# Kernel optimization log

Measured on AMD Instinct MI355X. Metric: run time of the kernel, lower is better.

Reference implementation:

```python
import jax, jax.numpy as jnp
import numpy as np

H = 8  # GRU hidden size (Dimension)


def _gru_last_hidden(x, Wih, Whh, bih, bhh):
    """Torch-style GRU (batch_first), returns final hidden state [B, H].
    x: [B, T, In]; Wih: [3H, In]; Whh: [3H, H]; bih, bhh: [3H].
    Gate order (torch): r, z, n.
    """
    B = x.shape[0]
    # precompute input projections for all timesteps: [B, T, 3H]
    xg = jnp.einsum('bti,gi->btg', x, Wih) + bih

    def step(h, xt):  # h: [B,H], xt: [B,3H]
        gh = h @ Whh.T + bhh  # [B, 3H]
        xr, xz, xn = jnp.split(xt, 3, axis=-1)
        hr, hz, hn = jnp.split(gh, 3, axis=-1)
        r = jax.nn.sigmoid(xr + hr)
        z = jax.nn.sigmoid(xz + hz)
        n = jnp.tanh(xn + r * hn)
        h_new = (1.0 - z) * n + z * h
        return h_new, None

    h0 = jnp.zeros((B, H), dtype=x.dtype)
    hT, _ = jax.lax.scan(step, h0, jnp.swapaxes(xg, 0, 1))  # scan over T
    return hT


def setup_inputs() -> dict:
    key = jax.random.key(0)
    ks = jax.random.split(key, 10)
    B, T = 1024, 512
    s = 0.2  # param init scale ~ 1/sqrt(H)*... small
    return {
        'bbox': jax.random.normal(ks[0], (B, T, 4), dtype=jnp.float32),
        'flow': jax.random.normal(ks[1], (B, T, 5, 5, 2), dtype=jnp.float32),
        'Wih_b': jax.random.normal(ks[2], (3 * H, 4), dtype=jnp.float32) * s,
        'Whh_b': jax.random.normal(ks[3], (3 * H, H), dtype=jnp.float32) * s,
        'bih_b': jax.random.normal(ks[4], (3 * H,), dtype=jnp.float32) * s,
        'bhh_b': jax.random.normal(ks[5], (3 * H,), dtype=jnp.float32) * s,
        'Wih_f': jax.random.normal(ks[6], (3 * H, 2), dtype=jnp.float32) * s,
        'Whh_f': jax.random.normal(ks[7], (3 * H, H), dtype=jnp.float32) * s,
        'bih_f': jax.random.normal(ks[8], (3 * H,), dtype=jnp.float32) * s,
        'bhh_f': jax.random.normal(ks[9], (3 * H,), dtype=jnp.float32) * s,
    }


def reference(bbox, flow, Wih_b, Whh_b, bih_b, bhh_b, Wih_f, Whh_f, bih_f, bhh_f):
    # vectorized equivalent of the triple Python loop: take center pixel
    storage = flow[:, :, 2, 2, :]  # [B, T, 2]
    h_bbox = _gru_last_hidden(bbox, Wih_b, Whh_b, bih_b, bhh_b)      # [B, H]
    h_flow = _gru_last_hidden(storage, Wih_f, Whh_f, bih_f, bhh_f)   # [B, H]
    feature = (h_bbox + h_flow) * 0.5
    return feature
```

## Files before the change

kernel.cpp:

```cpp
#include <hip/hip_runtime.h>

#define HDIM 8

__device__ __forceinline__ float ex2(float x) {
#if __has_builtin(__builtin_amdgcn_exp2f)
    return __builtin_amdgcn_exp2f(x);
#else
    return exp2f(x);
#endif
}
__device__ __forceinline__ float rcp(float x) {
#if __has_builtin(__builtin_amdgcn_rcpf)
    return __builtin_amdgcn_rcpf(x);
#else
    return 1.0f / x;
#endif
}

#define DPP_ROR(v, N)                                                        \
    __int_as_float(__builtin_amdgcn_update_dpp(                              \
        0, __float_as_int(v), 0x120 + (N), 0xF, 0xF, true))

template <int IN, int STRIDE>
__device__ float gru_elem(const float* __restrict__ xbase, int T,
                          const float* __restrict__ Wih, const float* __restrict__ Whh,
                          const float* __restrict__ bih, const float* __restrict__ bhh,
                          int j)
{
    const float NL2E = -1.4426950408889634f;
    const float L2E2 =  2.8853900817779268f;

    float nbp = DPP_ROR((float)j, 2);
    const int dstep = (nbp == (float)((j + 1) & 7)) ? 1 : 7;

    float wr[8], wz[8], wn[8];
#pragma unroll
    for (int m = 0; m < 8; ++m) {
        const int k = (j + dstep * m) & 7;
        wr[m] = NL2E * Whh[(j     ) * HDIM + k];
        wz[m] = NL2E * Whh[(j +  8) * HDIM + k];
        wn[m] = L2E2 * Whh[(j + 16) * HDIM + k];
    }
    float uir[IN], uiz[IN], uin[IN];
#pragma unroll
    for (int i = 0; i < IN; ++i) {
        uir[i] = NL2E * Wih[(j     ) * IN + i];
        uiz[i] = NL2E * Wih[(j +  8) * IN + i];
        uin[i] = L2E2 * Wih[(j + 16) * IN + i];
    }
    const float br  = NL2E * (bih[j]     + bhh[j]);
    const float bz  = NL2E * (bih[j + 8] + bhh[j + 8]);
    const float bn  = L2E2 * bih[j + 16];
    const float bhn = L2E2 * bhh[j + 16];

    constexpr int U = 8;
    float xb[U][IN];
    float pr[U], pz[U], pn[U];

    auto loadx = [&](const float* px) {
#pragma unroll
        for (int s = 0; s < U; ++s) {
            const float* p = px + s * STRIDE;
            if constexpr (IN == 4) {
                float4 v = *reinterpret_cast<const float4*>(p);
                xb[s][0] = v.x; xb[s][1] = v.y; xb[s][2] = v.z; xb[s][3] = v.w;
            } else {
                float2 v = *reinterpret_cast<const float2*>(p);
                xb[s][0] = v.x; xb[s][1] = v.y;
            }
        }
    };
    auto proj = [&]() {
#pragma unroll
        for (int s = 0; s < U; ++s) {
            float a = br, b = bz, c = bn;
#pragma unroll
            for (int i = 0; i < IN; ++i) {
                a = fmaf(uir[i], xb[s][i], a);
                b = fmaf(uiz[i], xb[s][i], b);
                c = fmaf(uin[i], xb[s][i], c);
            }
            pr[s] = a; pz[s] = b; pn[s] = c;
        }
    };

    const float* px = xbase;
    loadx(px);
    proj();
    px += U * STRIDE;
    float hj = 0.0f;

    for (int t0 = 0; t0 < T; t0 += U) {
        if (t0 + U < T) {
            loadx(px);
            px += U * STRIDE;
        }
#pragma unroll
        for (int s = 0; s < U; ++s) {
            const float hx0 = hj;
            const float hx1 = DPP_ROR(hj,  2);
            const float hx2 = DPP_ROR(hj,  4);
            const float hx3 = DPP_ROR(hj,  6);
            const float hx4 = DPP_ROR(hj,  8);
            const float hx5 = DPP_ROR(hj, 10);
            const float hx6 = DPP_ROR(hj, 12);
            const float hx7 = DPP_ROR(hj, 14);

            float ra = fmaf(wr[3], hx3, fmaf(wr[2], hx2, fmaf(wr[1], hx1, fmaf(wr[0], hx0, pr[s]))));
            float rb = fmaf(wr[7], hx7, fmaf(wr[6], hx6, fmaf(wr[5], hx5, wr[4] * hx4)));
            float za = fmaf(wz[3], hx3, fmaf(wz[2], hx2, fmaf(wz[1], hx1, fmaf(wz[0], hx0, pz[s]))));
            float zb = fmaf(wz[7], hx7, fmaf(wz[6], hx6, fmaf(wz[5], hx5, wz[4] * hx4)));
            float na = fmaf(wn[3], hx3, fmaf(wn[2], hx2, fmaf(wn[1], hx1, fmaf(wn[0], hx0, bhn))));
            float nb2 = fmaf(wn[7], hx7, fmaf(wn[6], hx6, fmaf(wn[5], hx5, wn[4] * hx4)));
            float sr = ra + rb;
            float sz = za + zb;
            float sn = na + nb2;

            float r = rcp(1.0f + ex2(sr));
            float z = rcp(1.0f + ex2(sz));
            float u = fmaf(r, sn, pn[s]);
            float n = fmaf(-2.0f, rcp(1.0f + ex2(u)), 1.0f);
            hj = fmaf(z, hj - n, n);
        }
        proj();
    }
    return hj;
}

__global__ __launch_bounds__(128, 1)
void gru_fused_kernel(const float* __restrict__ bbox, const float* __restrict__ flow,
                      const float* __restrict__ Wih_b, const float* __restrict__ Whh_b,
                      const float* __restrict__ bih_b, const float* __restrict__ bhh_b,
                      const float* __restrict__ Wih_f, const float* __restrict__ Whh_f,
                      const float* __restrict__ bih_f, const float* __restrict__ bhh_f,
                      float* __restrict__ out, int T)
{
    const int tid   = threadIdx.x;
    const int wave  = tid >> 6;
    const int lane  = tid & 63;
    const int eloc  = ((lane >> 4) << 1) | (lane & 1);
    const int j     = (lane & 15) >> 1;
    const int e     = blockIdx.x * 8 + eloc;

    __shared__ float sh[2][8][HDIM];

    float hT;
    if (wave == 0) {
        const float* xb = bbox + (size_t)e * T * 4;
        hT = gru_elem<4, 4>(xb, T, Wih_b, Whh_b, bih_b, bhh_b, j);
    } else {
        const float* xf = flow + (size_t)e * T * 50 + 24;
        hT = gru_elem<2, 50>(xf, T, Wih_f, Whh_f, bih_f, bhh_f, j);
    }

    sh[wave][eloc][j] = hT;
    __syncthreads();
    if (wave == 0) {
        out[(size_t)e * HDIM + j] = 0.5f * (sh[0][eloc][j] + sh[1][eloc][j]);
    }
}

extern "C" void kernel_launch(void* const* d_in, const int* in_sizes, int n_in,
                              void* d_out, int out_size, void* d_ws, size_t ws_size,
                              hipStream_t stream) {
    const float* bbox  = (const float*)d_in[0];
    const float* flow  = (const float*)d_in[1];
    const float* Wih_b = (const float*)d_in[2];
    const float* Whh_b = (const float*)d_in[3];
    const float* bih_b = (const float*)d_in[4];
    const float* bhh_b = (const float*)d_in[5];
    const float* Wih_f = (const float*)d_in[6];
    const float* Whh_f = (const float*)d_in[7];
    const float* bih_f = (const float*)d_in[8];
    const float* bhh_f = (const float*)d_in[9];
    float* out = (float*)d_out;

    const int B = out_size / HDIM;
    const int T = in_sizes[0] / (4 * B);

    dim3 grid(B / 8), block(128);
    gru_fused_kernel<<<grid, block, 0, stream>>>(
        bbox, flow, Wih_b, Whh_b, bih_b, bhh_b,
        Wih_f, Whh_f, bih_f, bhh_f, out, T);
}
```

Measured before the change: 68.62 us.

## Split GRU into producer waves for input projections and consumer waves for recurrence

Adds two producer waves per block that load the inputs and compute the input-gate projections for chunks of 16 timesteps. They write these into double-buffered LDS, and the two consumer waves read them while running the serial recurrence. The aim is to take global-memory latency and projection math off the recurrence's critical path. The trade-offs are a block barrier every chunk, twice as many threads per block, and extra LDS traffic. The code also assumes T is divisible by the chunk size.

```diff
diff --git a/kernel.cpp b/kernel.cpp
--- a/kernel.cpp
+++ b/kernel.cpp
@@ -1,6 +1,7 @@
 #include <hip/hip_runtime.h>
 
 #define HDIM 8
+#define CHUNK 16
 
 __device__ __forceinline__ float ex2(float x) {
 #if __has_builtin(__builtin_amdgcn_exp2f)
@@ -21,113 +22,90 @@
     __int_as_float(__builtin_amdgcn_update_dpp(                              \
         0, __float_as_int(v), 0x120 + (N), 0xF, 0xF, true))
 
+
 template <int IN, int STRIDE>
-__device__ float gru_elem(const float* __restrict__ xbase, int T,
-                          const float* __restrict__ Wih, const float* __restrict__ Whh,
-                          const float* __restrict__ bih, const float* __restrict__ bhh,
-                          int j)
+__device__ __forceinline__ void produce_chunk(
+    const float* __restrict__ xb, int t0,
+    const float (&uir)[8][4], const float (&uiz)[8][4], const float (&uin)[8][4],
+    const float (&cr)[8], const float (&cz)[8], const float (&cn)[8],
+    float* dst, int el, int q)
 {
-    const float NL2E = -1.4426950408889634f;
-    const float L2E2 =  2.8853900817779268f;
-
-    float nbp = DPP_ROR((float)j, 2);
-    const int dstep = (nbp == (float)((j + 1) & 7)) ? 1 : 7;
-
-    float wr[8], wz[8], wn[8];
-#pragma unroll
-    for (int m = 0; m < 8; ++m) {
-        const int k = (j + dstep * m) & 7;
-        wr[m] = NL2E * Whh[(j     ) * HDIM + k];
-        wz[m] = NL2E * Whh[(j +  8) * HDIM + k];
-        wn[m] = L2E2 * Whh[(j + 16) * HDIM + k];
-    }
-    float uir[IN], uiz[IN], uin[IN];
-#pragma unroll
-    for (int i = 0; i < IN; ++i) {
-        uir[i] = NL2E * Wih[(j     ) * IN + i];
-        uiz[i] = NL2E * Wih[(j +  8) * IN + i];
-        uin[i] = L2E2 * Wih[(j + 16) * IN + i];
-    }
-    const float br  = NL2E * (bih[j]     + bhh[j]);
-    const float bz  = NL2E * (bih[j + 8] + bhh[j + 8]);
-    const float bn  = L2E2 * bih[j + 16];
-    const float bhn = L2E2 * bhh[j + 16];
-
-    constexpr int U = 8;
-    float xb[U][IN];
-    float pr[U], pz[U], pn[U];
-
-    auto loadx = [&](const float* px) {
-#pragma unroll
-        for (int s = 0; s < U; ++s) {
-            const float* p = px + s * STRIDE;
-            if constexpr (IN == 4) {
-                float4 v = *reinterpret_cast<const float4*>(p);
-                xb[s][0] = v.x; xb[s][1] = v.y; xb[s][2] = v.z; xb[s][3] = v.w;
-            } else {
-                float2 v = *reinterpret_cast<const float2*>(p);
-                xb[s][0] = v.x; xb[s][1] = v.y;
+#pragma unroll
+    for (int h = 0; h < 2; ++h) {
+        const int s = q + 8 * h;
+        const float* p = xb + (size_t)(t0 + s) * STRIDE;
+        float x[IN];
+        if constexpr (IN == 4) {
+            float4 v = *reinterpret_cast<const float4*>(p);
+            x[0] = v.x; x[1] = v.y; x[2] = v.z; x[3] = v.w;
+        } else {
+            float2 v = *reinterpret_cast<const float2*>(p);
+            x[0] = v.x; x[1] = v.y;
+        }
+#pragma unroll
+        for (int jj = 0; jj < 8; ++jj) {
+            float a = cr[jj], b = cz[jj], c = cn[jj];
+#pragma unroll
+            for (int i = 0; i < IN; ++i) {
+                a = fmaf(uir[jj][i], x[i], a);
+                b = fmaf(uiz[jj][i], x[i], b);
+                c = fmaf(uin[jj][i], x[i], c);
             }
-        }
-    };
-    auto proj = [&]() {
-#pragma unroll
-        for (int s = 0; s < U; ++s) {
-            float a = br, b = bz, c = bn;
-#pragma unroll
-            for (int i = 0; i < IN; ++i) {
-                a = fmaf(uir[i], xb[s][i], a);
-                b = fmaf(uiz[i], xb[s][i], b);
-                c = fmaf(uin[i], xb[s][i], c);
-            }
-            pr[s] = a; pz[s] = b; pn[s] = c;
-        }
-    };
-
-    const float* px = xbase;
-    loadx(px);
-    proj();
-    px += U * STRIDE;
-    float hj = 0.0f;
-
-    for (int t0 = 0; t0 < T; t0 += U) {
-        if (t0 + U < T) {
-            loadx(px);
-            px += U * STRIDE;
-        }
-#pragma unroll
-        for (int s = 0; s < U; ++s) {
-            const float hx0 = hj;
-            const float hx1 = DPP_ROR(hj,  2);
-            const float hx2 = DPP_ROR(hj,  4);
-            const float hx3 = DPP_ROR(hj,  6);
-            const float hx4 = DPP_ROR(hj,  8);
-            const float hx5 = DPP_ROR(hj, 10);
-            const float hx6 = DPP_ROR(hj, 12);
-            const float hx7 = DPP_ROR(hj, 14);
-
-            float ra = fmaf(wr[3], hx3, fmaf(wr[2], hx2, fmaf(wr[1], hx1, fmaf(wr[0], hx0, pr[s]))));
-            float rb = fmaf(wr[7], hx7, fmaf(wr[6], hx6, fmaf(wr[5], hx5, wr[4] * hx4)));
-            float za = fmaf(wz[3], hx3, fmaf(wz[2], hx2, fmaf(wz[1], hx1, fmaf(wz[0], hx0, pz[s]))));
-            float zb = fmaf(wz[7], hx7, fmaf(wz[6], hx6, fmaf(wz[5], hx5, wz[4] * hx4)));
-            float na = fmaf(wn[3], hx3, fmaf(wn[2], hx2, fmaf(wn[1], hx1, fmaf(wn[0], hx0, bhn))));
-            float nb2 = fmaf(wn[7], hx7, fmaf(wn[6], hx6, fmaf(wn[5], hx5, wn[4] * hx4)));
-            float sr = ra + rb;
-            float sz = za + zb;
-            float sn = na + nb2;
-
-            float r = rcp(1.0f + ex2(sr));
-            float z = rcp(1.0f + ex2(sz));
-            float u = fmaf(r, sn, pn[s]);
-            float n = fmaf(-2.0f, rcp(1.0f + ex2(u)), 1.0f);
-            hj = fmaf(z, hj - n, n);
-        }
-        proj();
+            *reinterpret_cast<float4*>(dst + (size_t)(s * 8 + el) * 32 + jj * 4)
+                = make_float4(a, b, c, 0.0f);
+        }
+    }
+}
+
+__device__ __forceinline__ float consume_chunk(
+    float hj, const float* __restrict__ src, int el, int j,
+    const float (&wr)[8], const float (&wz)[8], const float (&wn)[8], float bhn)
+{
+    float4 pf[3];
+    pf[0] = *reinterpret_cast<const float4*>(src + (size_t)(0 * 8 + el) * 32 + j * 4);
+    pf[1] = *reinterpret_cast<const float4*>(src + (size_t)(1 * 8 + el) * 32 + j * 4);
+#pragma unroll
+    for (int s = 0; s < CHUNK; ++s) {
+        if (s + 2 < CHUNK)
+            pf[(s + 2) % 3] = *reinterpret_cast<const float4*>(
+                src + (size_t)((s + 2) * 8 + el) * 32 + j * 4);
+        const float4 P = pf[s % 3];
+
+        const float hx0 = hj;
+        const float hx1 = DPP_ROR(hj,  2);
+        const float hx2 = DPP_ROR(hj,  4);
+        const float hx3 = DPP_ROR(hj,  6);
+        const float hx4 = DPP_ROR(hj,  8);
+        const float hx5 = DPP_ROR(hj, 10);
+        const float hx6 = DPP_ROR(hj, 12);
+        const float hx7 = DPP_ROR(hj, 14);
+
+        float r01 = fmaf(wr[1], hx1, fmaf(wr[0], hx0, P.x));
+        float r23 = fmaf(wr[3], hx3, wr[2] * hx2);
+        float r45 = fmaf(wr[5], hx5, wr[4] * hx4);
+        float r67 = fmaf(wr[7], hx7, wr[6] * hx6);
+        float z01 = fmaf(wz[1], hx1, fmaf(wz[0], hx0, P.y));
+        float z23 = fmaf(wz[3], hx3, wz[2] * hx2);
+        float z45 = fmaf(wz[5], hx5, wz[4] * hx4);
+        float z67 = fmaf(wz[7], hx7, wz[6] * hx6);
+        float n01 = fmaf(wn[1], hx1, fmaf(wn[0], hx0, bhn));
+        float n23 = fmaf(wn[3], hx3, wn[2] * hx2);
+        float n45 = fmaf(wn[5], hx5, wn[4] * hx4);
+        float n67 = fmaf(wn[7], hx7, wn[6] * hx6);
+        float sr = (r01 + r23) + (r45 + r67);
+        float sz = (z01 + z23) + (z45 + z67);
+        float sn = (n01 + n23) + (n45 + n67);
+
+        float r = rcp(1.0f + ex2(sr));
+        float z = rcp(1.0f + ex2(sz));
+        float u = fmaf(r, sn, P.z);
+        float n = fmaf(-2.0f, rcp(1.0f + ex2(u)), 1.0f);
+        hj = fmaf(z, hj - n, n);
     }
     return hj;
 }
 
-__global__ __launch_bounds__(128, 1)
+__global__ __launch_bounds__(256, 1)
 void gru_fused_kernel(const float* __restrict__ bbox, const float* __restrict__ flow,
                       const float* __restrict__ Wih_b, const float* __restrict__ Whh_b,
                       const float* __restrict__ bih_b, const float* __restrict__ bhh_b,
@@ -135,27 +113,88 @@
                       const float* __restrict__ bih_f, const float* __restrict__ bhh_f,
                       float* __restrict__ out, int T)
 {
-    const int tid   = threadIdx.x;
-    const int wave  = tid >> 6;
-    const int lane  = tid & 63;
-    const int eloc  = ((lane >> 4) << 1) | (lane & 1);
-    const int j     = (lane & 15) >> 1;
-    const int e     = blockIdx.x * 8 + eloc;
-
+    const float NL2E = -1.4426950408889634f;
+    const float L2E2 =  2.8853900817779268f;
+
+    __shared__ float projLDS[2][2][CHUNK][8][32];
     __shared__ float sh[2][8][HDIM];
 
-    float hT;
-    if (wave == 0) {
-        const float* xb = bbox + (size_t)e * T * 4;
-        hT = gru_elem<4, 4>(xb, T, Wih_b, Whh_b, bih_b, bhh_b, j);
+    const int tid  = threadIdx.x;
+    const int wave = tid >> 6;
+    const int lane = tid & 63;
+    const int gru  = wave & 1;
+    const bool is_cons = (wave < 2);
+    const int NC = T / CHUNK;
+
+    const int eloc = ((lane >> 4) << 1) | (lane & 1);
+    const int j    = (lane & 15) >> 1;
+    float wr[8], wz[8], wn[8];
+    float bhn = 0.0f;
+
+    float uir[8][4], uiz[8][4], uin[8][4], cr[8], cz[8], cn[8];
+    const float* pxb = nullptr;
+    const int pel = lane >> 3;
+    const int pq  = lane & 7;
+
+    if (is_cons) {
+        const float* Whh = gru ? Whh_f : Whh_b;
+        const float* bhh = gru ? bhh_f : bhh_b;
+        float nbp = DPP_ROR((float)j, 2);
+        const int dstep = (nbp == (float)((j + 1) & 7)) ? 1 : 7;
+#pragma unroll
+        for (int m = 0; m < 8; ++m) {
+            const int k = (j + dstep * m) & 7;
+            wr[m] = NL2E * Whh[(j     ) * HDIM + k];
+            wz[m] = NL2E * Whh[(j +  8) * HDIM + k];
+            wn[m] = L2E2 * Whh[(j + 16) * HDIM + k];
+        }
+        bhn = L2E2 * bhh[j + 16];
     } else {
-        const float* xf = flow + (size_t)e * T * 50 + 24;
-        hT = gru_elem<2, 50>(xf, T, Wih_f, Whh_f, bih_f, bhh_f, j);
-    }
-
-    sh[wave][eloc][j] = hT;
+        const float* Wih = gru ? Wih_f : Wih_b;
+        const float* bih = gru ? bih_f : bih_b;
+        const float* bhh = gru ? bhh_f : bhh_b;
+        const int IN = gru ? 2 : 4;
+        const int pe = blockIdx.x * 8 + pel;
+        pxb = gru ? (flow + (size_t)pe * T * 50 + 24)
+                  : (bbox + (size_t)pe * T * 4);
+#pragma unroll
+        for (int jj = 0; jj < 8; ++jj) {
+            for (int i = 0; i < 4; ++i) { uir[jj][i] = 0.f; uiz[jj][i] = 0.f; uin[jj][i] = 0.f; }
+            for (int i = 0; i < IN; ++i) {
+                uir[jj][i] = NL2E * Wih[(jj     ) * IN + i];
+                uiz[jj][i] = NL2E * Wih[(jj +  8) * IN + i];
+                uin[jj][i] = L2E2 * Wih[(jj + 16) * IN + i];
+            }
+            cr[jj] = NL2E * (bih[jj]     + bhh[jj]);
+            cz[jj] = NL2E * (bih[jj + 8] + bhh[jj + 8]);
+            cn[jj] = L2E2 * bih[jj + 16];
+        }
+    }
+
+    float hj = 0.0f;
+
+    if (!is_cons) {
+        float* dst = &projLDS[0][gru][0][0][0];
+        if (gru == 0) produce_chunk<4, 4 >(pxb, 0, uir, uiz, uin, cr, cz, cn, dst, pel, pq);
+        else          produce_chunk<2, 50>(pxb, 0, uir, uiz, uin, cr, cz, cn, dst, pel, pq);
+    }
+    __syncthreads();
+
+    for (int c = 0; c < NC; ++c) {
+        if (is_cons) {
+            hj = consume_chunk(hj, &projLDS[c & 1][gru][0][0][0], eloc, j, wr, wz, wn, bhn);
+        } else if (c + 1 < NC) {
+            float* dst = &projLDS[(c + 1) & 1][gru][0][0][0];
+            if (gru == 0) produce_chunk<4, 4 >(pxb, (c + 1) * CHUNK, uir, uiz, uin, cr, cz, cn, dst, pel, pq);
+            else          produce_chunk<2, 50>(pxb, (c + 1) * CHUNK, uir, uiz, uin, cr, cz, cn, dst, pel, pq);
+        }
+        __syncthreads();
+    }
+
+    if (is_cons) sh[gru][eloc][j] = hj;
     __syncthreads();
     if (wave == 0) {
+        const int e = blockIdx.x * 8 + eloc;
         out[(size_t)e * HDIM + j] = 0.5f * (sh[0][eloc][j] + sh[1][eloc][j]);
     }
 }
@@ -178,7 +217,7 @@
     const int B = out_size / HDIM;
     const int T = in_sizes[0] / (4 * B);
 
-    dim3 grid(B / 8), block(128);
+    dim3 grid(B / 8), block(256);
     gru_fused_kernel<<<grid, block, 0, stream>>>(
         bbox, flow, Wih_b, Whh_b, bih_b, bhh_b,
         Wih_f, Whh_f, bih_f, bhh_f, out, T);
```

After: 81.18 us. 18.3% more time.

## Fuse DPP rotations into FMAs via inline asm and reorder gate math

Applied to the files above, without the earlier changes.

Replaces the separate DPP move plus FMA per hidden-state neighbour with v_mul_f32_dpp and v_fmac_f32_dpp inline asm, removing the extra move instructions on the serial recurrence critical path. The gate computation is reordered so the r gate's exp starts early, and the final blend is algebraically rewritten to shorten the dependency chain. Input loads become double-buffered A/B register sets with a 16-step loop, and the input projection is computed per step instead of batched. Weight setup is hoisted out of the templated body. The volatile asm limits compiler scheduling, and the loop assumes T is a multiple of 16.

```diff
diff --git a/kernel.cpp b/kernel.cpp
--- a/kernel.cpp
+++ b/kernel.cpp
@@ -1,6 +1,10 @@
 #include <hip/hip_runtime.h>
+#include <type_traits>
 
 #define HDIM 8
+
+typedef float v4f __attribute__((ext_vector_type(4)));
+typedef float v2f __attribute__((ext_vector_type(2)));
 
 __device__ __forceinline__ float ex2(float x) {
 #if __has_builtin(__builtin_amdgcn_exp2f)
@@ -21,108 +25,116 @@
     __int_as_float(__builtin_amdgcn_update_dpp(                              \
         0, __float_as_int(v), 0x120 + (N), 0xF, 0xF, true))
 
+#define ASM_FMA(d, a, b, c)                                                  \
+    asm volatile("v_fma_f32 %0, %1, %2, %3"                                  \
+                 : "=v"(d) : "v"(a), "v"(b), "v"(c))
+#define ASM_MULD(d, h, w, ROT)                                               \
+    asm volatile("v_mul_f32_dpp %0, %1, %2 row_ror:" #ROT                    \
+                 " row_mask:0xf bank_mask:0xf"                               \
+                 : "=v"(d) : "v"(h), "v"(w))
+#define ASM_FMACD(d, h, w, ROT)                                              \
+    asm volatile("v_fmac_f32_dpp %0, %1, %2 row_ror:" #ROT                   \
+                 " row_mask:0xf bank_mask:0xf"                               \
+                 : "+v"(d) : "v"(h), "v"(w))
+
+#define MEMBAR asm volatile("" ::: "memory")
+
+__device__ __forceinline__ float gru_step(float hj, v4f P,
+    const float (&wr)[8], const float (&wz)[8], const float (&wn)[8], float bhn)
+{
+    float ra, rb, na, nb, za, zb;
+    ASM_FMA (ra, wr[0], hj, P.x);
+    ASM_FMA (na, wn[0], hj, bhn);
+    ASM_MULD(rb, hj, wr[4], 8);
+    ASM_MULD(nb, hj, wn[4], 8);
+    ASM_FMACD(ra, hj, wr[1], 2);   ASM_FMACD(na, hj, wn[1], 2);
+    ASM_FMACD(rb, hj, wr[5], 10);  ASM_FMACD(nb, hj, wn[5], 10);
+    ASM_FMACD(ra, hj, wr[2], 4);   ASM_FMACD(na, hj, wn[2], 4);
+    ASM_FMACD(rb, hj, wr[6], 12);  ASM_FMACD(nb, hj, wn[6], 12);
+    ASM_FMACD(ra, hj, wr[3], 6);   ASM_FMACD(na, hj, wn[3], 6);
+    ASM_FMACD(rb, hj, wr[7], 14);  ASM_FMACD(nb, hj, wn[7], 14);
+    const float ar = ra + rb;
+    const float Er = ex2(ar);
+    ASM_FMA (za, wz[0], hj, P.y);
+    ASM_MULD(zb, hj, wz[4], 8);
+    ASM_FMACD(za, hj, wz[1], 2);
+    ASM_FMACD(zb, hj, wz[5], 10);
+    ASM_FMACD(za, hj, wz[2], 4);
+    ASM_FMACD(zb, hj, wz[6], 12);
+    ASM_FMACD(za, hj, wz[3], 6);
+    ASM_FMACD(zb, hj, wz[7], 14);
+    const float an_ = na + nb;
+    const float r  = rcp(1.0f + Er);
+    const float az = za + zb;
+    const float Ez = ex2(az);
+    const float u  = fmaf(r, an_, P.z);
+    const float En = ex2(u);
+    const float z  = rcp(1.0f + Ez);
+    const float q   = z * hj;
+    const float oz  = Ez * z;
+    const float s1  = q + oz;
+    const float m2o = -2.0f * oz;
+    const float rn  = rcp(1.0f + En);
+    return fmaf(rn, m2o, s1);
+}
+
 template <int IN, int STRIDE>
-__device__ float gru_elem(const float* __restrict__ xbase, int T,
-                          const float* __restrict__ Wih, const float* __restrict__ Whh,
-                          const float* __restrict__ bih, const float* __restrict__ bhh,
-                          int j)
+__device__ __forceinline__ float gru_run(
+    const float* __restrict__ px, int T,
+    const float (&ur)[4], const float (&uz)[4], const float (&un)[4],
+    float cr, float cz, float cn,
+    const float (&wr)[8], const float (&wz)[8], const float (&wn)[8], float bhn)
 {
-    const float NL2E = -1.4426950408889634f;
-    const float L2E2 =  2.8853900817779268f;
-
-    float nbp = DPP_ROR((float)j, 2);
-    const int dstep = (nbp == (float)((j + 1) & 7)) ? 1 : 7;
-
-    float wr[8], wz[8], wn[8];
+    using vx = std::conditional_t<IN == 4, v4f, v2f>;
+    auto LD = [&](int t) -> vx {
+        return *reinterpret_cast<const vx*>(px + (size_t)t * STRIDE);
+    };
+    auto PROJ = [&](vx x) -> v4f {
+        float a = cr, b = cz, c = cn;
 #pragma unroll
-    for (int m = 0; m < 8; ++m) {
-        const int k = (j + dstep * m) & 7;
-        wr[m] = NL2E * Whh[(j     ) * HDIM + k];
-        wz[m] = NL2E * Whh[(j +  8) * HDIM + k];
-        wn[m] = L2E2 * Whh[(j + 16) * HDIM + k];
-    }
-    float uir[IN], uiz[IN], uin[IN];
-#pragma unroll
-    for (int i = 0; i < IN; ++i) {
-        uir[i] = NL2E * Wih[(j     ) * IN + i];
-        uiz[i] = NL2E * Wih[(j +  8) * IN + i];
-        uin[i] = L2E2 * Wih[(j + 16) * IN + i];
-    }
-    const float br  = NL2E * (bih[j]     + bhh[j]);
-    const float bz  = NL2E * (bih[j + 8] + bhh[j + 8]);
-    const float bn  = L2E2 * bih[j + 16];
-    const float bhn = L2E2 * bhh[j + 16];
-
-    constexpr int U = 8;
-    float xb[U][IN];
-    float pr[U], pz[U], pn[U];
-
-    auto loadx = [&](const float* px) {
-#pragma unroll
-        for (int s = 0; s < U; ++s) {
-            const float* p = px + s * STRIDE;
-            if constexpr (IN == 4) {
-                float4 v = *reinterpret_cast<const float4*>(p);
-                xb[s][0] = v.x; xb[s][1] = v.y; xb[s][2] = v.z; xb[s][3] = v.w;
-            } else {
-                float2 v = *reinterpret_cast<const float2*>(p);
-                xb[s][0] = v.x; xb[s][1] = v.y;
-            }
+        for (int i = 0; i < IN; ++i) {
+            a = fmaf(ur[i], x[i], a);
+            b = fmaf(uz[i], x[i], b);
+            c = fmaf(un[i], x[i], c);
         }
+        return v4f{a, b, c, 0.0f};
     };
-    auto proj = [&]() {
-#pragma unroll
-        for (int s = 0; s < U; ++s) {
-            float a = br, b = bz, c = bn;
-#pragma unroll
-            for (int i = 0; i < IN; ++i) {
-                a = fmaf(uir[i], xb[s][i], a);
-                b = fmaf(uiz[i], xb[s][i], b);
-                c = fmaf(uin[i], xb[s][i], c);
-            }
-            pr[s] = a; pz[s] = b; pn[s] = c;
+
+    vx A0, A1, A2, A3, A4, A5, A6, A7;
+    vx B0, B1, B2, B3, B4, B5, B6, B7;
+
+    A0 = LD(0); A1 = LD(1); A2 = LD(2); A3 = LD(3);
+    A4 = LD(4); A5 = LD(5); A6 = LD(6); A7 = LD(7);
+    MEMBAR;
+
+    float hj = 0.0f;
+    for (int t0 = 0; t0 < T; t0 += 16) {
+        if (t0 + 8 < T) {
+            B0 = LD(t0 + 8);  B1 = LD(t0 + 9);  B2 = LD(t0 + 10); B3 = LD(t0 + 11);
+            B4 = LD(t0 + 12); B5 = LD(t0 + 13); B6 = LD(t0 + 14); B7 = LD(t0 + 15);
         }
-    };
-
-    const float* px = xbase;
-    loadx(px);
-    proj();
-    px += U * STRIDE;
-    float hj = 0.0f;
-
-    for (int t0 = 0; t0 < T; t0 += U) {
-        if (t0 + U < T) {
-            loadx(px);
-            px += U * STRIDE;
+        MEMBAR;
+        hj = gru_step(hj, PROJ(A0), wr, wz, wn, bhn);
+        hj = gru_step(hj, PROJ(A1), wr, wz, wn, bhn);
+        hj = gru_step(hj, PROJ(A2), wr, wz, wn, bhn);
+        hj = gru_step(hj, PROJ(A3), wr, wz, wn, bhn);
+        hj = gru_step(hj, PROJ(A4), wr, wz, wn, bhn);
+        hj = gru_step(hj, PROJ(A5), wr, wz, wn, bhn);
+        hj = gru_step(hj, PROJ(A6), wr, wz, wn, bhn);
+        hj = gru_step(hj, PROJ(A7), wr, wz, wn, bhn);
+        if (t0 + 16 < T) {
+            A0 = LD(t0 + 16); A1 = LD(t0 + 17); A2 = LD(t0 + 18); A3 = LD(t0 + 19);
+            A4 = LD(t0 + 20); A5 = LD(t0 + 21); A6 = LD(t0 + 22); A7 = LD(t0 + 23);
         }
-#pragma unroll
-        for (int s = 0; s < U; ++s) {
-            const float hx0 = hj;
-            const float hx1 = DPP_ROR(hj,  2);
-            const float hx2 = DPP_ROR(hj,  4);
-            const float hx3 = DPP_ROR(hj,  6);
-            const float hx4 = DPP_ROR(hj,  8);
-            const float hx5 = DPP_ROR(hj, 10);
-            const float hx6 = DPP_ROR(hj, 12);
-            const float hx7 = DPP_ROR(hj, 14);
-
-            float ra = fmaf(wr[3], hx3, fmaf(wr[2], hx2, fmaf(wr[1], hx1, fmaf(wr[0], hx0, pr[s]))));
-            float rb = fmaf(wr[7], hx7, fmaf(wr[6], hx6, fmaf(wr[5], hx5, wr[4] * hx4)));
-            float za = fmaf(wz[3], hx3, fmaf(wz[2], hx2, fmaf(wz[1], hx1, fmaf(wz[0], hx0, pz[s]))));
-            float zb = fmaf(wz[7], hx7, fmaf(wz[6], hx6, fmaf(wz[5], hx5, wz[4] * hx4)));
-            float na = fmaf(wn[3], hx3, fmaf(wn[2], hx2, fmaf(wn[1], hx1, fmaf(wn[0], hx0, bhn))));
-            float nb2 = fmaf(wn[7], hx7, fmaf(wn[6], hx6, fmaf(wn[5], hx5, wn[4] * hx4)));
-            float sr = ra + rb;
-            float sz = za + zb;
-            float sn = na + nb2;
-
-            float r = rcp(1.0f + ex2(sr));
-            float z = rcp(1.0f + ex2(sz));
-            float u = fmaf(r, sn, pn[s]);
-            float n = fmaf(-2.0f, rcp(1.0f + ex2(u)), 1.0f);
-            hj = fmaf(z, hj - n, n);
-        }
-        proj();
+        MEMBAR;
+        hj = gru_step(hj, PROJ(B0), wr, wz, wn, bhn);
+        hj = gru_step(hj, PROJ(B1), wr, wz, wn, bhn);
+        hj = gru_step(hj, PROJ(B2), wr, wz, wn, bhn);
+        hj = gru_step(hj, PROJ(B3), wr, wz, wn, bhn);
+        hj = gru_step(hj, PROJ(B4), wr, wz, wn, bhn);
+        hj = gru_step(hj, PROJ(B5), wr, wz, wn, bhn);
+        hj = gru_step(hj, PROJ(B6), wr, wz, wn, bhn);
+        hj = gru_step(hj, PROJ(B7), wr, wz, wn, bhn);
     }
     return hj;
 }
@@ -135,22 +147,54 @@
                       const float* __restrict__ bih_f, const float* __restrict__ bhh_f,
                       float* __restrict__ out, int T)
 {
-    const int tid   = threadIdx.x;
-    const int wave  = tid >> 6;
-    const int lane  = tid & 63;
-    const int eloc  = ((lane >> 4) << 1) | (lane & 1);
-    const int j     = (lane & 15) >> 1;
-    const int e     = blockIdx.x * 8 + eloc;
+    const float NL2E = -1.4426950408889634f;
+    const float L2E2 =  2.8853900817779268f;
 
     __shared__ float sh[2][8][HDIM];
+
+    const int tid  = threadIdx.x;
+    const int wave = tid >> 6;
+    const int lane = tid & 63;
+    const int eloc = ((lane >> 4) << 1) | (lane & 1);
+    const int j    = (lane & 15) >> 1;
+    const int e    = blockIdx.x * 8 + eloc;
+
+    const float* Wih = wave ? Wih_f : Wih_b;
+    const float* Whh = wave ? Whh_f : Whh_b;
+    const float* bih = wave ? bih_f : bih_b;
+    const float* bhh = wave ? bhh_f : bhh_b;
+    const int IN = wave ? 2 : 4;
+
+    float nbp = DPP_ROR((float)j, 2);
+    const int dstep = (nbp == (float)((j + 1) & 7)) ? 1 : 7;
+
+    float wr[8], wz[8], wn[8];
+#pragma unroll
+    for (int m = 0; m < 8; ++m) {
+        const int k = (j + dstep * m) & 7;
+        wr[m] = NL2E * Whh[(j     ) * HDIM + k];
+        wz[m] = NL2E * Whh[(j +  8) * HDIM + k];
+        wn[m] = L2E2 * Whh[(j + 16) * HDIM + k];
+    }
+    const float bhn = L2E2 * bhh[j + 16];
+
+    float ur[4] = {0, 0, 0, 0}, uz[4] = {0, 0, 0, 0}, un[4] = {0, 0, 0, 0};
+    for (int i = 0; i < IN; ++i) {
+        ur[i] = NL2E * Wih[(j     ) * IN + i];
+        uz[i] = NL2E * Wih[(j +  8) * IN + i];
+        un[i] = L2E2 * Wih[(j + 16) * IN + i];
+    }
+    const float cr = NL2E * (bih[j]     + bhh[j]);
+    const float cz = NL2E * (bih[j + 8] + bhh[j + 8]);
+    const float cn = L2E2 * bih[j + 16];
 
     float hT;
     if (wave == 0) {
-        const float* xb = bbox + (size_t)e * T * 4;
-        hT = gru_elem<4, 4>(xb, T, Wih_b, Whh_b, bih_b, bhh_b, j);
+        const float* px = bbox + (size_t)e * T * 4;
+        hT = gru_run<4, 4>(px, T, ur, uz, un, cr, cz, cn, wr, wz, wn, bhn);
     } else {
-        const float* xf = flow + (size_t)e * T * 50 + 24;
-        hT = gru_elem<2, 50>(xf, T, Wih_f, Whh_f, bih_f, bhh_f, j);
+        const float* px = flow + (size_t)e * T * 50 + 24;
+        hT = gru_run<2, 50>(px, T, ur, uz, un, cr, cz, cn, wr, wz, wn, bhn);
     }
 
     sh[wave][eloc][j] = hT;
```

Measured after the change: 74.54 us. 8.6% more time.
